# Kernel tuning notes

Measured on AMD Instinct MI355X. Metric: run time of the kernel, lower is better.

Reference implementation:

```python
import jax, jax.numpy as jnp
import numpy as np

B, L, D, H = 4, 2048, 1024, 16
HD = D // H  # head_dim = 64


def setup_inputs() -> dict:
    key = jax.random.key(0)
    ks = jax.random.split(key, 13)
    s = 1.0 / np.sqrt(D)
    inp = {
        'q': jax.random.normal(ks[0], (B, L, D), jnp.float32),
        'k': jax.random.normal(ks[1], (B, L, D), jnp.float32),
        'v': jax.random.normal(ks[2], (B, L, D), jnp.float32),
        'mask': jax.random.randint(ks[3], (B, 1, L, L), 0, 2, jnp.int32),
        'WQ': jax.random.normal(ks[4], (D, D), jnp.float32) * s,
        'bQ': jnp.zeros((D,), jnp.float32),
        'WK': jax.random.normal(ks[5], (D, D), jnp.float32) * s,
        'bK': jnp.zeros((D,), jnp.float32),
        'WV': jax.random.normal(ks[6], (D, D), jnp.float32) * s,
        'bV': jnp.zeros((D,), jnp.float32),
        'WO': jax.random.normal(ks[7], (D, D), jnp.float32) * s,
        'bO': jnp.zeros((D,), jnp.float32),
    }
    return inp


def reference(q, k, v, mask, WQ, bQ, WK, bK, WV, bV, WO, bO):
    # Linear projections (torch Linear: x @ W.T + b; here W stored as [D,D], use x @ W + b equivalently)
    Q = q @ WQ + bQ  # [B, L, D]
    K = k @ WK + bK
    V = v @ WV + bV
    # split heads -> [B, H, L, HD]
    Q = Q.reshape(B, L, H, HD).transpose(0, 2, 1, 3)
    K = K.reshape(B, L, H, HD).transpose(0, 2, 1, 3)
    V = V.reshape(B, L, H, HD).transpose(0, 2, 1, 3)
    scale = 1.0 / np.sqrt(HD).astype(np.float32)
    scores = jnp.einsum('bhqd,bhkd->bhqk', Q, K) * scale  # [B, H, Lq, Lk]
    scores = jnp.where(mask == 0, -jnp.inf, scores)  # mask broadcasts over heads
    attn = jax.nn.softmax(scores, axis=-1)
    # dropout p=0 (eval) -> identity
    ctx = jnp.einsum('bhqk,bhkd->bhqd', attn, V)  # [B, H, L, HD]
    ctx = ctx.transpose(0, 2, 1, 3).reshape(B, L, D)
    return ctx @ WO + bO
```

## Files before the change

kernel.cpp:

```cpp
#include <hip/hip_runtime.h>
#include <math.h>

#define B_  4
#define L_  2048
#define D_  1024
#define H_  16
#define HD_ 64

typedef __attribute__((ext_vector_type(8))) short short8;
typedef __attribute__((ext_vector_type(4))) float f32x4;
typedef __attribute__((ext_vector_type(16))) float f32x16;
typedef __attribute__((ext_vector_type(4))) int   i32x4;

__device__ static inline unsigned short f2bf(float f) {
    union { float f; unsigned int u; } v; v.f = f;
    const unsigned int u = v.u;
    return (unsigned short)((u + 0x7FFFu + ((u >> 16) & 1u)) >> 16);
}

__device__ static inline unsigned cvt_pk_bf16(float a, float b) {
    unsigned r;
    asm("v_cvt_pk_bf16_f32 %0, %1, %2" : "=v"(r) : "v"(a), "v"(b));
    return r;
}

__device__ static inline void async_copy16(const void* g, void* lds)
{
    __builtin_amdgcn_global_load_lds(
        (const __attribute__((address_space(1))) void*)g,
        (__attribute__((address_space(3))) void*)lds, 16, 0, 0);
}

__global__ __launch_bounds__(256) void cvt3_bf16_kernel(
    const float* __restrict__ i0, const float* __restrict__ i1,
    const float* __restrict__ i2,
    unsigned short* __restrict__ o0, unsigned short* __restrict__ o1,
    unsigned short* __restrict__ o2)
{
    const float* in = blockIdx.y == 0 ? i0 : blockIdx.y == 1 ? i1 : i2;
    unsigned short* out = blockIdx.y == 0 ? o0 : blockIdx.y == 1 ? o1 : o2;
    const size_t i = ((size_t)blockIdx.x * 256 + threadIdx.x) * 8;
    const float4 x = *(const float4*)&in[i];
    const float4 y = *(const float4*)&in[i + 4];
    ushort4 a0, a1;
    a0.x = f2bf(x.x); a0.y = f2bf(x.y); a0.z = f2bf(x.z); a0.w = f2bf(x.w);
    a1.x = f2bf(y.x); a1.y = f2bf(y.y); a1.z = f2bf(y.z); a1.w = f2bf(y.w);
    *(ushort4*)&out[i]     = a0;
    *(ushort4*)&out[i + 4] = a1;
}

__global__ __launch_bounds__(256) void transpose_bf16_kernel(
    const float* __restrict__ W, unsigned short* __restrict__ WT)
{
    __shared__ float t[32][33];
    const int c  = threadIdx.x & 31;
    const int r8 = threadIdx.x >> 5;
    const int k0 = blockIdx.y * 32;
    const int n0 = blockIdx.x * 32;
    #pragma unroll
    for (int i = 0; i < 4; ++i) {
        const int r = r8 + i * 8;
        t[r][c] = W[(size_t)(k0 + r) * 1024 + n0 + c];
    }
    __syncthreads();
    #pragma unroll
    for (int i = 0; i < 4; ++i) {
        const int r = r8 + i * 8;
        WT[(size_t)(n0 + r) * 1024 + k0 + c] = f2bf(t[c][r]);
    }
}

__global__ __launch_bounds__(256) void trans3_bf16_kernel(
    const float* __restrict__ W0, const float* __restrict__ W1,
    const float* __restrict__ W2,
    unsigned short* __restrict__ T0, unsigned short* __restrict__ T1,
    unsigned short* __restrict__ T2)
{
    __shared__ float t[32][33];
    const float* W = blockIdx.z == 0 ? W0 : blockIdx.z == 1 ? W1 : W2;
    unsigned short* WT = blockIdx.z == 0 ? T0 : blockIdx.z == 1 ? T1 : T2;
    const int c  = threadIdx.x & 31;
    const int r8 = threadIdx.x >> 5;
    const int k0 = blockIdx.y * 32;
    const int n0 = blockIdx.x * 32;
    #pragma unroll
    for (int i = 0; i < 4; ++i) {
        const int r = r8 + i * 8;
        t[r][c] = W[(size_t)(k0 + r) * 1024 + n0 + c];
    }
    __syncthreads();
    #pragma unroll
    for (int i = 0; i < 4; ++i) {
        const int r = r8 + i * 8;
        WT[(size_t)(n0 + r) * 1024 + k0 + c] = f2bf(t[c][r]);
    }
}

__global__ __launch_bounds__(256) void vtrans_bf16_kernel(
    const unsigned short* __restrict__ Vb, unsigned short* __restrict__ vtb)
{
    __shared__ unsigned short t[64][68];
    const int tid = threadIdx.x;
    const int l0  = blockIdx.x * 64;
    const int h   = blockIdx.y;
    const int b   = blockIdx.z;
    const int rr  = tid >> 4;
    const int c4  = (tid & 15) * 4;
    #pragma unroll
    for (int i = 0; i < 4; ++i) {
        const int r = i * 16 + rr;
        *(ushort4*)&t[r][c4] =
            *(const ushort4*)&Vb[((size_t)(b * L_ + l0 + r)) * D_ + h * 64 + c4];
    }
    __syncthreads();
    #pragma unroll
    for (int i = 0; i < 4; ++i) {
        const int d = i * 16 + rr;
        ushort4 o;
        o.x = t[c4 + 0][d]; o.y = t[c4 + 1][d];
        o.z = t[c4 + 2][d]; o.w = t[c4 + 3][d];
        *(ushort4*)&vtb[((size_t)((b * H_ + h) * 64 + d)) * L_ + l0 + c4] = o;
    }
}

__global__ __launch_bounds__(256) void pack_mask32_kernel(
    const int* __restrict__ mask, unsigned int* __restrict__ mm)
{
    const unsigned g = blockIdx.x * 256 + threadIdx.x;
    const int v = mask[g];
    const unsigned long long bm = __ballot(v != 0);
    const int lane = threadIdx.x & 63;
    const int b = g >> 22;
    const int q = (g >> 11) & 2047;
    const int k = g & 2047;
    const unsigned idx = ((unsigned)(b * 32 + (k >> 6)) * 2048 + q) * 2 + ((k >> 5) & 1);
    if (lane == 0)       mm[idx] = (unsigned)bm;
    else if (lane == 32) mm[idx] = (unsigned)(bm >> 32);
}

template<int OUT_BF16>
__device__ static inline void gemm_body(
    const unsigned short* __restrict__ A, const unsigned short* __restrict__ WT,
    const float* __restrict__ bias, void* __restrict__ Cv,
    int M, int N, int K, float omul,
    unsigned short* At, unsigned short* Bt)
{
    const int tid  = threadIdx.x;
    const int lane = tid & 63;
    const int wave = tid >> 6;
    const int wm   = wave >> 1;
    const int wn   = wave & 1;
    const int quad = lane >> 4;
    const int l15  = lane & 15;
    const int m0   = blockIdx.y * 128;
    const int n0   = blockIdx.x * 128;

    f32x4 acc[4][4];
    #pragma unroll
    for (int i = 0; i < 4; ++i)
        #pragma unroll
        for (int j = 0; j < 4; ++j) acc[i][j] = (f32x4)0.f;

    for (int k0 = 0; k0 < K; k0 += 64) {
        __syncthreads();
        #pragma unroll
        for (int i = 0; i < 4; ++i) {
            const int fb  = i * 256 + wave * 64;
            const int f   = fb + lane;
            const int row = f >> 3;
            const int c8  = f & 7;
            async_copy16(&A [(size_t)(m0 + row) * K + k0 + c8 * 8],
                         (char*)At + (size_t)fb * 16);
            async_copy16(&WT[(size_t)(n0 + row) * K + k0 + c8 * 8],
                         (char*)Bt + (size_t)fb * 16);
        }
        __syncthreads();

        #pragma unroll
        for (int kk = 0; kk < 64; kk += 32) {
            short8 afr[4], bfr[4];
            #pragma unroll
            for (int mt = 0; mt < 4; ++mt)
                afr[mt] = *(const short8*)&At[(size_t)(wm * 64 + mt * 16 + l15) * 64 + kk + quad * 8];
            #pragma unroll
            for (int nt = 0; nt < 4; ++nt)
                bfr[nt] = *(const short8*)&Bt[(size_t)(wn * 64 + nt * 16 + l15) * 64 + kk + quad * 8];
            __builtin_amdgcn_s_setprio(1);
            #pragma unroll
            for (int mt = 0; mt < 4; ++mt)
                #pragma unroll
                for (int nt = 0; nt < 4; ++nt)
                    acc[mt][nt] = __builtin_amdgcn_mfma_f32_16x16x32_bf16(
                        afr[mt], bfr[nt], acc[mt][nt], 0, 0, 0);
            __builtin_amdgcn_s_setprio(0);
        }
    }

    #pragma unroll
    for (int nt = 0; nt < 4; ++nt) {
        const int col = n0 + wn * 64 + nt * 16 + l15;
        const float bv = bias[col];
        #pragma unroll
        for (int mt = 0; mt < 4; ++mt) {
            const int r0 = m0 + wm * 64 + mt * 16 + quad * 4;
            #pragma unroll
            for (int r = 0; r < 4; ++r) {
                const float val = (acc[mt][nt][r] + bv) * omul;
                if constexpr (OUT_BF16)
                    ((unsigned short*)Cv)[(size_t)(r0 + r) * N + col] = f2bf(val);
                else
                    ((float*)Cv)[(size_t)(r0 + r) * N + col] = val;
            }
        }
    }
}

__global__ __launch_bounds__(256) void gemm3_mfma_kernel(
    const unsigned short* __restrict__ A0, const unsigned short* __restrict__ A1,
    const unsigned short* __restrict__ A2,
    const unsigned short* __restrict__ W0, const unsigned short* __restrict__ W1,
    const unsigned short* __restrict__ W2,
    const float* __restrict__ b0, const float* __restrict__ b1,
    const float* __restrict__ b2,
    unsigned short* __restrict__ C0, unsigned short* __restrict__ C1,
    unsigned short* __restrict__ C2, float om0)
{
    __shared__ __align__(16) unsigned short At[128 * 64];
    __shared__ __align__(16) unsigned short Bt[128 * 64];
    const int z = blockIdx.z;
    const unsigned short* A  = z == 0 ? A0 : z == 1 ? A1 : A2;
    const unsigned short* WT = z == 0 ? W0 : z == 1 ? W1 : W2;
    const float* bias        = z == 0 ? b0 : z == 1 ? b1 : b2;
    unsigned short* C        = z == 0 ? C0 : z == 1 ? C1 : C2;
    const float omul         = z == 0 ? om0 : 1.f;
    gemm_body<1>(A, WT, bias, C, B_ * L_, D_, D_, omul, At, Bt);
}

__global__ __launch_bounds__(256) void gemm_mfma_kernel(
    const unsigned short* __restrict__ A, const unsigned short* __restrict__ WT,
    const float* __restrict__ bias, float* __restrict__ C,
    int M, int N, int K)
{
    __shared__ __align__(16) unsigned short At[128 * 64];
    __shared__ __align__(16) unsigned short Bt[128 * 64];
    gemm_body<0>(A, WT, bias, C, M, N, K, 1.f, At, Bt);
}

#define AQ 128
#define AK 64
#define NT (L_ / AK)

__global__ __launch_bounds__(256, 4) void attn_mfma_kernel(
    const unsigned short* __restrict__ Qb,
    const unsigned short* __restrict__ Kb,
    const unsigned short* __restrict__ Vtg,
    const unsigned int* __restrict__ mbt,
    unsigned short* __restrict__ Cb)
{
    __shared__ __align__(16) unsigned short Kt[2][AK * 64];
    __shared__ __align__(16) unsigned short Vs[2][64 * AK];
    __shared__ __align__(16) unsigned int   Mt[2][AQ * 2];

    const int tid  = threadIdx.x;
    const int lane = tid & 63;
    const int w    = tid >> 6;
    const int hi   = lane >> 5;
    const int l31  = lane & 31;

    const int nid = (blockIdx.x & 7) * 128 + (blockIdx.x >> 3);
    const int q0  = (nid & 15) * AQ;
    const int h   = (nid >> 4) & 15;
    const int b   = nid >> 8;

    const unsigned short* kbase = &Kb [((size_t)(b * L_)) * D_ + h * 64];
    const unsigned short* vbase = &Vtg[((size_t)((b * H_ + h) * 64)) * L_];
    const unsigned int*   mbase = &mbt[((size_t)(b * 32) * 2048 + q0) * 2];

    const int q = q0 + w * 32 + l31;

    short8 qf[4];
    #pragma unroll
    for (int ds = 0; ds < 4; ++ds)
        qf[ds] = *(const short8*)
            &Qb[((size_t)(b * L_ + q)) * D_ + h * 64 + ds * 16 + hi * 8];

    f32x16 ot[2];
    ot[0] = (f32x16)0.f; ot[1] = (f32x16)0.f;
    float m_run = -INFINITY, l_run = 0.f;

    const int swz = l31 & 7;

    auto stage = [&](int bi, int kt) {
        const int k0 = kt * AK;
        #pragma unroll
        for (int i = 0; i < 2; ++i) {
            const int fb = i * 256 + w * 64;
            const int f  = fb + lane;
            const int r  = f >> 3;
            const int cs = (f & 7) ^ (r & 7);
            async_copy16(&kbase[(size_t)(k0 + r) * D_ + cs * 8],
                         (char*)&Kt[bi][0] + fb * 16);
            async_copy16(&vbase[(size_t)r * L_ + k0 + cs * 8],
                         (char*)&Vs[bi][0] + fb * 16);
        }
        if (w == 3)
            async_copy16(&mbase[(size_t)kt * 2048 * 2 + lane * 4],
                         (char*)&Mt[bi][0]);
    };

    stage(0, 0);
    __syncthreads();

    for (int kt = 0; kt < NT; ++kt) {
        const int cur = kt & 1;
        if (kt + 1 < NT) stage(cur ^ 1, kt + 1);

        f32x16 st0, st1;
        {
            short8 kf0 = *(const short8*)
                &Kt[cur][(l31) * 64 + ((0 * 2 + hi) ^ swz) * 8];
            short8 kf1 = *(const short8*)
                &Kt[cur][(32 + l31) * 64 + ((0 * 2 + hi) ^ swz) * 8];
            __builtin_amdgcn_s_setprio(1);
            st0 = __builtin_amdgcn_mfma_f32_32x32x16_bf16(
                kf0, qf[0], (f32x16)0.f, 0, 0, 0);
            st1 = __builtin_amdgcn_mfma_f32_32x32x16_bf16(
                kf1, qf[0], (f32x16)0.f, 0, 0, 0);
            __builtin_amdgcn_s_setprio(0);
        }
        #pragma unroll
        for (int ds = 1; ds < 4; ++ds) {
            short8 kf0 = *(const short8*)
                &Kt[cur][(l31) * 64 + ((ds * 2 + hi) ^ swz) * 8];
            short8 kf1 = *(const short8*)
                &Kt[cur][(32 + l31) * 64 + ((ds * 2 + hi) ^ swz) * 8];
            __builtin_amdgcn_s_setprio(1);
            st0 = __builtin_amdgcn_mfma_f32_32x32x16_bf16(
                kf0, qf[ds], st0, 0, 0, 0);
            st1 = __builtin_amdgcn_mfma_f32_32x32x16_bf16(
                kf1, qf[ds], st1, 0, 0, 0);
            __builtin_amdgcn_s_setprio(0);
        }

        const uint2 mm = *(const uint2*)&Mt[cur][(w * 32 + l31) * 2];
        float rmax = -INFINITY;
        #pragma unroll
        for (int kr = 0; kr < 2; ++kr) {
            const unsigned w32 = kr ? mm.y : mm.x;
            #pragma unroll
            for (int s = 0; s < 4; ++s) {
                const unsigned nib = (w32 >> (s * 8 + hi * 4)) & 0xFu;
                #pragma unroll
                for (int r = 0; r < 4; ++r) {
                    float x = kr ? st1[s * 4 + r] : st0[s * 4 + r];
                    x = ((nib >> r) & 1u) ? x : -INFINITY;
                    if (kr) st1[s * 4 + r] = x; else st0[s * 4 + r] = x;
                    rmax = fmaxf(rmax, x);
                }
            }
        }
        rmax = fmaxf(rmax, __shfl_xor(rmax, 32));
        if (__any(rmax > m_run + 8.f)) {
            const float mnew  = fmaxf(m_run, rmax);
            const float alpha = __builtin_amdgcn_exp2f(
                m_run - fmaxf(mnew, -1e30f));
            l_run *= alpha;
            #pragma unroll
            for (int db = 0; db < 2; ++db)
                #pragma unroll
                for (int i = 0; i < 16; ++i) ot[db][i] *= alpha;
            m_run = mnew;
        }
        const float msafe = fmaxf(m_run, -1e30f);
        float psum = 0.f;
        #pragma unroll
        for (int kr = 0; kr < 2; ++kr)
            #pragma unroll
            for (int i = 0; i < 16; ++i) {
                const float p = __builtin_amdgcn_exp2f(
                    (kr ? st1[i] : st0[i]) - msafe);
                if (kr) st1[i] = p; else st0[i] = p;
                psum += p;
            }
        psum += __shfl_xor(psum, 32);
        l_run += psum;

        #pragma unroll
        for (int ks = 0; ks < 4; ++ks) {
            const int sA = (ks & 1) * 2;
            short8 vf0 = *(const short8*)
                &Vs[cur][(l31) * 64 + ((ks * 2 + hi) ^ swz) * 8];
            short8 vf1 = *(const short8*)
                &Vs[cur][(32 + l31) * 64 + ((ks * 2 + hi) ^ swz) * 8];
            unsigned cLo0, cLo1, cHi0, cHi1;
            if (ks >> 1) {
                cLo0 = cvt_pk_bf16(st1[sA*4+0], st1[sA*4+1]);
                cLo1 = cvt_pk_bf16(st1[sA*4+2], st1[sA*4+3]);
                cHi0 = cvt_pk_bf16(st1[sA*4+4], st1[sA*4+5]);
                cHi1 = cvt_pk_bf16(st1[sA*4+6], st1[sA*4+7]);
            } else {
                cLo0 = cvt_pk_bf16(st0[sA*4+0], st0[sA*4+1]);
                cLo1 = cvt_pk_bf16(st0[sA*4+2], st0[sA*4+3]);
                cHi0 = cvt_pk_bf16(st0[sA*4+4], st0[sA*4+5]);
                cHi1 = cvt_pk_bf16(st0[sA*4+6], st0[sA*4+7]);
            }
            const int xLo0 = __shfl_xor((int)cLo0, 32);
            const int xLo1 = __shfl_xor((int)cLo1, 32);
            const int xHi0 = __shfl_xor((int)cHi0, 32);
            const int xHi1 = __shfl_xor((int)cHi1, 32);
            i32x4 t;
            t.x = hi ? xHi0 : (int)cLo0;
            t.y = hi ? xHi1 : (int)cLo1;
            t.z = hi ? (int)cHi0 : xLo0;
            t.w = hi ? (int)cHi1 : xLo1;
            const short8 pf = *reinterpret_cast<short8*>(&t);
            __builtin_amdgcn_s_setprio(1);
            ot[0] = __builtin_amdgcn_mfma_f32_32x32x16_bf16(
                vf0, pf, ot[0], 0, 0, 0);
            ot[1] = __builtin_amdgcn_mfma_f32_32x32x16_bf16(
                vf1, pf, ot[1], 0, 0, 0);
            __builtin_amdgcn_s_setprio(0);
        }

        __syncthreads();
    }

    const float rinv = (l_run > 0.f) ? (1.f / l_run) : 0.f;
    const size_t base = ((size_t)(b * L_ + q)) * D_ + h * 64;
    #pragma unroll
    for (int db = 0; db < 2; ++db)
        #pragma unroll
        for (int s = 0; s < 4; ++s) {
            ushort4 o;
            o.x = f2bf(ot[db][s * 4 + 0] * rinv);
            o.y = f2bf(ot[db][s * 4 + 1] * rinv);
            o.z = f2bf(ot[db][s * 4 + 2] * rinv);
            o.w = f2bf(ot[db][s * 4 + 3] * rinv);
            *(ushort4*)&Cb[base + db * 32 + s * 8 + hi * 4] = o;
        }
}

extern "C" void kernel_launch(void* const* d_in, const int* in_sizes, int n_in,
                              void* d_out, int out_size, void* d_ws, size_t ws_size,
                              hipStream_t stream)
{
    const float* q    = (const float*)d_in[0];
    const float* k    = (const float*)d_in[1];
    const float* v    = (const float*)d_in[2];
    const int*   mask = (const int*)d_in[3];
    const float* WQ   = (const float*)d_in[4];
    const float* bQ   = (const float*)d_in[5];
    const float* WK   = (const float*)d_in[6];
    const float* bK   = (const float*)d_in[7];
    const float* WV   = (const float*)d_in[8];
    const float* bV   = (const float*)d_in[9];
    const float* WO   = (const float*)d_in[10];
    const float* bO   = (const float*)d_in[11];
    float* out = (float*)d_out;

    const size_t NTOK = (size_t)B_ * L_;

    char* W = (char*)d_ws;
    unsigned short* qin = (unsigned short*)(W);
    unsigned short* kin = (unsigned short*)(W + ((size_t)16  << 20));
    unsigned short* vin = (unsigned short*)(W + ((size_t)32  << 20));
    unsigned short* qbf = (unsigned short*)(W + ((size_t)48  << 20));
    unsigned short* kbf = (unsigned short*)(W + ((size_t)64  << 20));
    unsigned short* vbf = (unsigned short*)(W + ((size_t)80  << 20));
    unsigned short* vtb = (unsigned short*)(W + ((size_t)96  << 20));
    unsigned short* cb  = (unsigned short*)(W + ((size_t)112 << 20));
    unsigned short* WTo = vin;

    unsigned int*   mbt32 = (unsigned int*)d_out;
    unsigned short* WTq = (unsigned short*)((char*)d_out + ((size_t)2 << 20));
    unsigned short* WTk = (unsigned short*)((char*)d_out + ((size_t)4 << 20));
    unsigned short* WTv = (unsigned short*)((char*)d_out + ((size_t)6 << 20));

    pack_mask32_kernel<<<(B_ * L_ * L_) / 256, 256, 0, stream>>>(mask, mbt32);

    const int cvtg = (int)(NTOK * D_ / (256 * 8));
    cvt3_bf16_kernel<<<dim3(cvtg, 3), 256, 0, stream>>>(q, k, v, qin, kin, vin);

    trans3_bf16_kernel<<<dim3(32, 32, 3), 256, 0, stream>>>(
        WQ, WK, WV, WTq, WTk, WTv);

    const float qscale = 0.125f * 1.44269504088896340736f;
    dim3 ggrd3(D_ / 128, NTOK / 128, 3);
    gemm3_mfma_kernel<<<ggrd3, 256, 0, stream>>>(
        qin, kin, vin, WTq, WTk, WTv, bQ, bK, bV, qbf, kbf, vbf, qscale);

    transpose_bf16_kernel<<<dim3(32, 32), 256, 0, stream>>>(WO, WTo);
    vtrans_bf16_kernel<<<dim3(L_ / 64, H_, B_), 256, 0, stream>>>(vbf, vtb);

    attn_mfma_kernel<<<dim3(1024), 256, 0, stream>>>(qbf, kbf, vtb, mbt32, cb);

    dim3 ggrd(D_ / 128, NTOK / 128);
    gemm_mfma_kernel<<<ggrd, 256, 0, stream>>>(cb, WTo, bO, out, (int)NTOK, D_, D_);
}
```

Before: 480.2 us.

## Fuse V transpose into projection GEMM and software-pipeline QK across attention tiles

Result: slower. 747.6 us (+55.7%).

```diff
diff --git a/kernel.cpp b/kernel.cpp
--- a/kernel.cpp
+++ b/kernel.cpp
@@ -96,33 +96,6 @@
     }
 }
 
-__global__ __launch_bounds__(256) void vtrans_bf16_kernel(
-    const unsigned short* __restrict__ Vb, unsigned short* __restrict__ vtb)
-{
-    __shared__ unsigned short t[64][68];
-    const int tid = threadIdx.x;
-    const int l0  = blockIdx.x * 64;
-    const int h   = blockIdx.y;
-    const int b   = blockIdx.z;
-    const int rr  = tid >> 4;
-    const int c4  = (tid & 15) * 4;
-    #pragma unroll
-    for (int i = 0; i < 4; ++i) {
-        const int r = i * 16 + rr;
-        *(ushort4*)&t[r][c4] =
-            *(const ushort4*)&Vb[((size_t)(b * L_ + l0 + r)) * D_ + h * 64 + c4];
-    }
-    __syncthreads();
-    #pragma unroll
-    for (int i = 0; i < 4; ++i) {
-        const int d = i * 16 + rr;
-        ushort4 o;
-        o.x = t[c4 + 0][d]; o.y = t[c4 + 1][d];
-        o.z = t[c4 + 2][d]; o.w = t[c4 + 3][d];
-        *(ushort4*)&vtb[((size_t)((b * H_ + h) * 64 + d)) * L_ + l0 + c4] = o;
-    }
-}
-
 __global__ __launch_bounds__(256) void pack_mask32_kernel(
     const int* __restrict__ mask, unsigned int* __restrict__ mm)
 {
@@ -142,7 +115,7 @@
 __device__ static inline void gemm_body(
     const unsigned short* __restrict__ A, const unsigned short* __restrict__ WT,
     const float* __restrict__ bias, void* __restrict__ Cv,
-    int M, int N, int K, float omul,
+    int M, int N, int K, float omul, int vmode,
     unsigned short* At, unsigned short* Bt)
 {
     const int tid  = threadIdx.x;
@@ -196,6 +169,28 @@
         }
     }
 
+    if (OUT_BF16 && vmode) {
+        #pragma unroll
+        for (int nt = 0; nt < 4; ++nt) {
+            const int col = n0 + wn * 64 + nt * 16 + l15;
+            const float bv = bias[col];
+            const int hh = col >> 6, dl = col & 63;
+            #pragma unroll
+            for (int mt = 0; mt < 4; ++mt) {
+                const int m  = m0 + wm * 64 + mt * 16 + quad * 4;
+                const int bb = m >> 11, ll = m & 2047;
+                ushort4 o;
+                o.x = f2bf(acc[mt][nt][0] + bv);
+                o.y = f2bf(acc[mt][nt][1] + bv);
+                o.z = f2bf(acc[mt][nt][2] + bv);
+                o.w = f2bf(acc[mt][nt][3] + bv);
+                *(ushort4*)&((unsigned short*)Cv)[
+                    ((size_t)(bb * H_ + hh) * 64 + dl) * 2048 + ll] = o;
+            }
+        }
+        return;
+    }
+
     #pragma unroll
     for (int nt = 0; nt < 4; ++nt) {
         const int col = n0 + wn * 64 + nt * 16 + l15;
@@ -233,7 +228,7 @@
     const float* bias        = z == 0 ? b0 : z == 1 ? b1 : b2;
     unsigned short* C        = z == 0 ? C0 : z == 1 ? C1 : C2;
     const float omul         = z == 0 ? om0 : 1.f;
-    gemm_body<1>(A, WT, bias, C, B_ * L_, D_, D_, omul, At, Bt);
+    gemm_body<1>(A, WT, bias, C, B_ * L_, D_, D_, omul, z == 2, At, Bt);
 }
 
 __global__ __launch_bounds__(256) void gemm_mfma_kernel(
@@ -243,7 +238,7 @@
 {
     __shared__ __align__(16) unsigned short At[128 * 64];
     __shared__ __align__(16) unsigned short Bt[128 * 64];
-    gemm_body<0>(A, WT, bias, C, M, N, K, 1.f, At, Bt);
+    gemm_body<0>(A, WT, bias, C, M, N, K, 1.f, 0, At, Bt);
 }
 
 #define AQ 128
@@ -259,7 +254,6 @@
 {
     __shared__ __align__(16) unsigned short Kt[2][AK * 64];
     __shared__ __align__(16) unsigned short Vs[2][64 * AK];
-    __shared__ __align__(16) unsigned int   Mt[2][AQ * 2];
 
     const int tid  = threadIdx.x;
     const int lane = tid & 63;
@@ -274,9 +268,9 @@
 
     const unsigned short* kbase = &Kb [((size_t)(b * L_)) * D_ + h * 64];
     const unsigned short* vbase = &Vtg[((size_t)((b * H_ + h) * 64)) * L_];
-    const unsigned int*   mbase = &mbt[((size_t)(b * 32) * 2048 + q0) * 2];
 
     const int q = q0 + w * 32 + l31;
+    const unsigned int* mrow = &mbt[((size_t)(b * 32) * 2048 + q) * 2];
 
     short8 qf[4];
     #pragma unroll
@@ -290,7 +284,7 @@
 
     const int swz = l31 & 7;
 
-    auto stage = [&](int bi, int kt) {
+    auto stageK = [&](int bi, int kt) {
         const int k0 = kt * AK;
         #pragma unroll
         for (int i = 0; i < 2; ++i) {
@@ -300,61 +294,59 @@
             const int cs = (f & 7) ^ (r & 7);
             async_copy16(&kbase[(size_t)(k0 + r) * D_ + cs * 8],
                          (char*)&Kt[bi][0] + fb * 16);
+        }
+    };
+    auto stageV = [&](int bi, int kt) {
+        const int k0 = kt * AK;
+        #pragma unroll
+        for (int i = 0; i < 2; ++i) {
+            const int fb = i * 256 + w * 64;
+            const int f  = fb + lane;
+            const int r  = f >> 3;
+            const int cs = (f & 7) ^ (r & 7);
             async_copy16(&vbase[(size_t)r * L_ + k0 + cs * 8],
                          (char*)&Vs[bi][0] + fb * 16);
         }
-        if (w == 3)
-            async_copy16(&mbase[(size_t)kt * 2048 * 2 + lane * 4],
-                         (char*)&Mt[bi][0]);
     };
 
-    stage(0, 0);
-    __syncthreads();
-
-    for (int kt = 0; kt < NT; ++kt) {
-        const int cur = kt & 1;
-        if (kt + 1 < NT) stage(cur ^ 1, kt + 1);
-
-        f32x16 st0, st1;
-        {
+    auto qk = [&](int bi, f32x16& D0, f32x16& D1) {
+        #pragma unroll
+        for (int ds = 0; ds < 4; ++ds) {
             short8 kf0 = *(const short8*)
-                &Kt[cur][(l31) * 64 + ((0 * 2 + hi) ^ swz) * 8];
+                &Kt[bi][(l31) * 64 + ((ds * 2 + hi) ^ swz) * 8];
             short8 kf1 = *(const short8*)
-                &Kt[cur][(32 + l31) * 64 + ((0 * 2 + hi) ^ swz) * 8];
+                &Kt[bi][(32 + l31) * 64 + ((ds * 2 + hi) ^ swz) * 8];
             __builtin_amdgcn_s_setprio(1);
-            st0 = __builtin_amdgcn_mfma_f32_32x32x16_bf16(
-                kf0, qf[0], (f32x16)0.f, 0, 0, 0);
-            st1 = __builtin_amdgcn_mfma_f32_32x32x16_bf16(
-                kf1, qf[0], (f32x16)0.f, 0, 0, 0);
+            D0 = __builtin_amdgcn_mfma_f32_32x32x16_bf16(
+                kf0, qf[ds], ds ? D0 : (f32x16)0.f, 0, 0, 0);
+            D1 = __builtin_amdgcn_mfma_f32_32x32x16_bf16(
+                kf1, qf[ds], ds ? D1 : (f32x16)0.f, 0, 0, 0);
             __builtin_amdgcn_s_setprio(0);
         }
-        #pragma unroll
-        for (int ds = 1; ds < 4; ++ds) {
-            short8 kf0 = *(const short8*)
-                &Kt[cur][(l31) * 64 + ((ds * 2 + hi) ^ swz) * 8];
-            short8 kf1 = *(const short8*)
-                &Kt[cur][(32 + l31) * 64 + ((ds * 2 + hi) ^ swz) * 8];
-            __builtin_amdgcn_s_setprio(1);
-            st0 = __builtin_amdgcn_mfma_f32_32x32x16_bf16(
-                kf0, qf[ds], st0, 0, 0, 0);
-            st1 = __builtin_amdgcn_mfma_f32_32x32x16_bf16(
-                kf1, qf[ds], st1, 0, 0, 0);
-            __builtin_amdgcn_s_setprio(0);
-        }
-
-        const uint2 mm = *(const uint2*)&Mt[cur][(w * 32 + l31) * 2];
+    };
+
+    f32x16 stA0, stA1, stB0, stB1;
+
+    auto body = [&](int t, f32x16& P0, f32x16& P1, f32x16& N0, f32x16& N1) {
+        stageK(t & 1,      (t + 2 < NT) ? t + 2 : NT - 1);
+        stageV((t + 1) & 1, (t + 1 < NT) ? t + 1 : NT - 1);
+        const uint2 mm = *(const uint2*)&mrow[(size_t)t * 4096];
+
+        qk((t + 1) & 1, N0, N1);
+
         float rmax = -INFINITY;
         #pragma unroll
         for (int kr = 0; kr < 2; ++kr) {
+            f32x16& S = kr ? P1 : P0;
             const unsigned w32 = kr ? mm.y : mm.x;
             #pragma unroll
             for (int s = 0; s < 4; ++s) {
                 const unsigned nib = (w32 >> (s * 8 + hi * 4)) & 0xFu;
                 #pragma unroll
                 for (int r = 0; r < 4; ++r) {
-                    float x = kr ? st1[s * 4 + r] : st0[s * 4 + r];
+                    float x = S[s * 4 + r];
                     x = ((nib >> r) & 1u) ? x : -INFINITY;
-                    if (kr) st1[s * 4 + r] = x; else st0[s * 4 + r] = x;
+                    S[s * 4 + r] = x;
                     rmax = fmaxf(rmax, x);
                 }
             }
@@ -374,46 +366,40 @@
         const float msafe = fmaxf(m_run, -1e30f);
         float psum = 0.f;
         #pragma unroll
-        for (int kr = 0; kr < 2; ++kr)
+        for (int kr = 0; kr < 2; ++kr) {
+            f32x16& S = kr ? P1 : P0;
             #pragma unroll
             for (int i = 0; i < 16; ++i) {
-                const float p = __builtin_amdgcn_exp2f(
-                    (kr ? st1[i] : st0[i]) - msafe);
-                if (kr) st1[i] = p; else st0[i] = p;
+                const float p = __builtin_amdgcn_exp2f(S[i] - msafe);
+                S[i] = p;
                 psum += p;
             }
+        }
         psum += __shfl_xor(psum, 32);
         l_run += psum;
 
         #pragma unroll
         for (int ks = 0; ks < 4; ++ks) {
             const int sA = (ks & 1) * 2;
+            f32x16& S = (ks >> 1) ? P1 : P0;
             short8 vf0 = *(const short8*)
-                &Vs[cur][(l31) * 64 + ((ks * 2 + hi) ^ swz) * 8];
+                &Vs[t & 1][(l31) * 64 + ((ks * 2 + hi) ^ swz) * 8];
             short8 vf1 = *(const short8*)
-                &Vs[cur][(32 + l31) * 64 + ((ks * 2 + hi) ^ swz) * 8];
-            unsigned cLo0, cLo1, cHi0, cHi1;
-            if (ks >> 1) {
-                cLo0 = cvt_pk_bf16(st1[sA*4+0], st1[sA*4+1]);
-                cLo1 = cvt_pk_bf16(st1[sA*4+2], st1[sA*4+3]);
-                cHi0 = cvt_pk_bf16(st1[sA*4+4], st1[sA*4+5]);
-                cHi1 = cvt_pk_bf16(st1[sA*4+6], st1[sA*4+7]);
-            } else {
-                cLo0 = cvt_pk_bf16(st0[sA*4+0], st0[sA*4+1]);
-                cLo1 = cvt_pk_bf16(st0[sA*4+2], st0[sA*4+3]);
-                cHi0 = cvt_pk_bf16(st0[sA*4+4], st0[sA*4+5]);
-                cHi1 = cvt_pk_bf16(st0[sA*4+6], st0[sA*4+7]);
-            }
+                &Vs[t & 1][(32 + l31) * 64 + ((ks * 2 + hi) ^ swz) * 8];
+            unsigned cLo0 = cvt_pk_bf16(S[sA*4+0], S[sA*4+1]);
+            unsigned cLo1 = cvt_pk_bf16(S[sA*4+2], S[sA*4+3]);
+            unsigned cHi0 = cvt_pk_bf16(S[sA*4+4], S[sA*4+5]);
+            unsigned cHi1 = cvt_pk_bf16(S[sA*4+6], S[sA*4+7]);
             const int xLo0 = __shfl_xor((int)cLo0, 32);
             const int xLo1 = __shfl_xor((int)cLo1, 32);
             const int xHi0 = __shfl_xor((int)cHi0, 32);
             const int xHi1 = __shfl_xor((int)cHi1, 32);
-            i32x4 t;
-            t.x = hi ? xHi0 : (int)cLo0;
-            t.y = hi ? xHi1 : (int)cLo1;
-            t.z = hi ? (int)cHi0 : xLo0;
-            t.w = hi ? (int)cHi1 : xLo1;
-            const short8 pf = *reinterpret_cast<short8*>(&t);
+            i32x4 tt;
+            tt.x = hi ? xHi0 : (int)cLo0;
+            tt.y = hi ? xHi1 : (int)cLo1;
+            tt.z = hi ? (int)cHi0 : xLo0;
+            tt.w = hi ? (int)cHi1 : xLo1;
+            const short8 pf = *reinterpret_cast<short8*>(&tt);
             __builtin_amdgcn_s_setprio(1);
             ot[0] = __builtin_amdgcn_mfma_f32_32x32x16_bf16(
                 vf0, pf, ot[0], 0, 0, 0);
@@ -423,6 +409,18 @@
         }
 
         __syncthreads();
+    };
+
+    stageK(0, 0);
+    stageV(0, 0);
+    stageK(1, 1);
+    __syncthreads();
+    qk(0, stA0, stA1);
+    __syncthreads();
+
+    for (int t = 0; t < NT; t += 2) {
+        body(t,     stA0, stA1, stB0, stB1);
+        body(t + 1, stB0, stB1, stA0, stA1);
     }
 
     const float rinv = (l_run > 0.f) ? (1.f / l_run) : 0.f;
@@ -466,9 +464,8 @@
     unsigned short* vin = (unsigned short*)(W + ((size_t)32  << 20));
     unsigned short* qbf = (unsigned short*)(W + ((size_t)48  << 20));
     unsigned short* kbf = (unsigned short*)(W + ((size_t)64  << 20));
-    unsigned short* vbf = (unsigned short*)(W + ((size_t)80  << 20));
-    unsigned short* vtb = (unsigned short*)(W + ((size_t)96  << 20));
-    unsigned short* cb  = (unsigned short*)(W + ((size_t)112 << 20));
+    unsigned short* vtb = (unsigned short*)(W + ((size_t)80  << 20));
+    unsigned short* cb  = (unsigned short*)(W + ((size_t)96  << 20));
     unsigned short* WTo = vin;
 
     unsigned int*   mbt32 = (unsigned int*)d_out;
@@ -487,10 +484,9 @@
     const float qscale = 0.125f * 1.44269504088896340736f;
     dim3 ggrd3(D_ / 128, NTOK / 128, 3);
     gemm3_mfma_kernel<<<ggrd3, 256, 0, stream>>>(
-        qin, kin, vin, WTq, WTk, WTv, bQ, bK, bV, qbf, kbf, vbf, qscale);
+        qin, kin, vin, WTq, WTk, WTv, bQ, bK, bV, qbf, kbf, vtb, qscale);
 
     transpose_bf16_kernel<<<dim3(32, 32), 256, 0, stream>>>(WO, WTo);
-    vtrans_bf16_kernel<<<dim3(L_ / 64, H_, B_), 256, 0, stream>>>(vbf, vtb);
 
     attn_mfma_kernel<<<dim3(1024), 256, 0, stream>>>(qbf, kbf, vtb, mbt32, cb);
 
```
